# Kernel tuning notes

Measured on AMD Instinct MI355X. Metric: run time of the kernel, lower is better.

## Reference

```python
import jax, jax.numpy as jnp
import numpy as np

N = 50000      # nodes
E = 600000     # edges
D = 128        # num_features == hidden_dim
H = 1          # heads (only runnable config of this module)
C = 128        # per-head channels
L = 2          # num_layers
G = 64         # graphs in batch
NC = 10        # num_classes


def setup_inputs() -> dict:
    key = jax.random.key(0)
    ks = jax.random.split(key, 12)
    s = 1.0 / np.sqrt(D)
    inp = {
        "x": jax.random.normal(ks[0], (N, D), jnp.float32),
        "edge_index": jax.random.randint(ks[1], (2, E), 0, N),
        "batch": jnp.sort(jax.random.randint(ks[2], (N,), 0, G)),
        # per-layer TransformerConv params (stacked over layers)
        "Wq": jax.random.normal(ks[3], (L, D, H * C), jnp.float32) * s,
        "bq": jax.random.normal(ks[4], (L, H * C), jnp.float32) * 0.01,
        "Wk": jax.random.normal(ks[5], (L, D, H * C), jnp.float32) * s,
        "bk": jax.random.normal(ks[6], (L, H * C), jnp.float32) * 0.01,
        "Wv": jax.random.normal(ks[7], (L, D, H * C), jnp.float32) * s,
        "bv": jax.random.normal(ks[8], (L, H * C), jnp.float32) * 0.01,
        "Ws": jax.random.normal(ks[9], (L, D, H * C), jnp.float32) * s,  # lin_skip (root weight)
        "bs": jax.random.normal(ks[10], (L, H * C), jnp.float32) * 0.01,
        "W_fc": jax.random.normal(ks[11], (H * C, NC), jnp.float32) * (1.0 / np.sqrt(H * C)),
        "b_fc": jnp.zeros((NC,), jnp.float32),
    }
    return inp


def _transformer_conv(x, src, dst, wq, bq, wk, bk, wv, bv, ws, bs):
    n = x.shape[0]
    q = (x @ wq + bq).reshape(n, H, C)
    k = (x @ wk + bk).reshape(n, H, C)
    v = (x @ wv + bv).reshape(n, H, C)
    # edge-wise gather: query from dst (x_i), key/value from src (x_j)
    score = (q[dst] * k[src]).sum(-1) / jnp.sqrt(jnp.float32(C))  # [E, H]
    # segment softmax over incoming edges of each dst node
    m = jax.ops.segment_max(score, dst, num_segments=n)           # [N, H]
    ex = jnp.exp(score - m[dst])
    den = jax.ops.segment_sum(ex, dst, num_segments=n)
    alpha = ex / den[dst]                                         # [E, H]
    agg = jax.ops.segment_sum(alpha[..., None] * v[src], dst, num_segments=n)
    return agg.reshape(n, H * C) + x @ ws + bs                    # concat heads + skip


def reference(x, edge_index, batch, Wq, bq, Wk, bk, Wv, bv, Ws, bs, W_fc, b_fc):
    src, dst = edge_index[0], edge_index[1]
    h = x
    for l in range(L):
        h = jax.nn.relu(_transformer_conv(h, src, dst, Wq[l], bq[l], Wk[l], bk[l],
                                          Wv[l], bv[l], Ws[l], bs[l]))
    # global mean pool per graph
    sums = jax.ops.segment_sum(h, batch, num_segments=G)
    cnts = jax.ops.segment_sum(jnp.ones((h.shape[0],), h.dtype), batch, num_segments=G)
    pooled = sums / jnp.maximum(cnts, 1.0)[:, None]
    logits = pooled @ W_fc + b_fc
    return jax.nn.log_softmax(logits, axis=1)
```

## Files before the change

### kernel.cpp

```cpp
#include <hip/hip_runtime.h>
#include <math.h>

#define NN 50000
#define EE 600000
#define DD 128
#define GG 64
#define NCLS 10
#define PCHUNK 64
#define NTILE (NN / 16)
#define NBUK 196
#define BSTRIDE 4096
#define EPB ((EE + 255) / 256)

typedef __attribute__((ext_vector_type(8))) __bf16 bf16x8;
typedef __attribute__((ext_vector_type(8))) unsigned short u16x8;
typedef __attribute__((ext_vector_type(4))) float f32x4;
typedef __attribute__((ext_vector_type(2))) float f32x2;

#define LGKM_FENCE() asm volatile("s_waitcnt lgkmcnt(0)" ::: "memory")
#define SCHED_FENCE() __builtin_amdgcn_sched_barrier(0)

__device__ __forceinline__ unsigned short f2bf(float f) {
    unsigned int u = __float_as_uint(f);
    u += 0x7fff + ((u >> 16) & 1);
    return (unsigned short)(u >> 16);
}

__device__ __forceinline__ float bf2f(unsigned short h) {
    return __uint_as_float(((unsigned int)h) << 16);
}

__device__ __forceinline__ float lo16(unsigned int u) { return __uint_as_float(u << 16); }
__device__ __forceinline__ float hi16(unsigned int u) { return __uint_as_float(u & 0xffff0000u); }


__global__ __launch_bounds__(256) void prep_kernel(
    const float* __restrict__ wq, const float* __restrict__ wk,
    const float* __restrict__ wv, const float* __restrict__ ws,
    const float* __restrict__ x, unsigned short* __restrict__ xb,
    unsigned short* __restrict__ wt,
    int* __restrict__ bucketcnt, float* __restrict__ gsum) {
    int tid = blockIdx.x * 256 + threadIdx.x;
    int TOT = gridDim.x * 256;
    if (tid < 256) bucketcnt[tid] = 0;
    for (int i = tid; i < GG * DD + GG; i += TOT) gsum[i] = 0.f;
    for (int i = tid; i < 2 * 4 * 16384; i += TOT) {
        int k = i & 127;
        int n = (i >> 7) & 127;
        int lm = i >> 14;
        int l = lm >> 2, m = lm & 3;
        const float* w = (m == 0) ? wq : (m == 1) ? wk : (m == 2) ? wv : ws;
        wt[i] = f2bf(w[l * 16384 + k * 128 + n]);
    }
    for (int i = tid; i < NN * DD / 8; i += TOT) {
        const float* px = x + (size_t)i * 8;
        float4 f0 = *(const float4*)px;
        float4 f1 = *(const float4*)(px + 4);
        u16x8 o;
        o[0] = f2bf(f0.x); o[1] = f2bf(f0.y); o[2] = f2bf(f0.z); o[3] = f2bf(f0.w);
        o[4] = f2bf(f1.x); o[5] = f2bf(f1.y); o[6] = f2bf(f1.z); o[7] = f2bf(f1.w);
        *(u16x8*)(xb + (size_t)i * 8) = o;
    }
}


__global__ __launch_bounds__(1024) void bucket_kernel(
    const int* __restrict__ src, const int* __restrict__ dst,
    int* __restrict__ bucketcnt, int2* __restrict__ bedge) {
    __shared__ int hist[256];
    __shared__ int base[256];
    int t = threadIdx.x;
    if (t < 256) hist[t] = 0;
    __syncthreads();
    int e0 = blockIdx.x * EPB;
    int eend = min(e0 + EPB, EE);

    int b0 = -1, b1 = -1, b2 = -1;
    int sl0 = 0, sl1 = 0, sl2 = 0;
    int s0 = 0, s1 = 0, s2 = 0, d0 = 0, d1 = 0, d2 = 0;
    int i = e0 + t;
    if (i < eend) { d0 = dst[i]; s0 = src[i]; b0 = d0 >> 8; sl0 = atomicAdd(&hist[b0], 1); }
    i += 1024;
    if (i < eend) { d1 = dst[i]; s1 = src[i]; b1 = d1 >> 8; sl1 = atomicAdd(&hist[b1], 1); }
    i += 1024;
    if (i < eend) { d2 = dst[i]; s2 = src[i]; b2 = d2 >> 8; sl2 = atomicAdd(&hist[b2], 1); }
    __syncthreads();

    if (t < 256) {
        int h = hist[t];
        base[t] = h ? atomicAdd(&bucketcnt[t], h) : 0;
    }
    __syncthreads();

    if (b0 >= 0) bedge[b0 * BSTRIDE + base[b0] + sl0] = make_int2(s0, d0);
    if (b1 >= 0) bedge[b1 * BSTRIDE + base[b1] + sl1] = make_int2(s1, d1);
    if (b2 >= 0) bedge[b2 * BSTRIDE + base[b2] + sl2] = make_int2(s2, d2);
}


__global__ __launch_bounds__(1024) void bsort_kernel(
    const int* __restrict__ bucketcnt, const int2* __restrict__ bedge,
    int* __restrict__ indptr, int* __restrict__ esrc) {
    __shared__ int buf[256];
    __shared__ int cur[256];
    int b = blockIdx.x;
    int t = threadIdx.x;

    if (t < 256) buf[t] = (t < NBUK) ? bucketcnt[t] : 0;
    __syncthreads();
    if (t < 64) {
        int carry = 0;
        #pragma unroll
        for (int c = 0; c < 4; ++c) {
            int v = buf[c * 64 + t];
            int x = v;
            #pragma unroll
            for (int off = 1; off < 64; off <<= 1) {
                int y = __shfl_up(x, off);
                if (t >= off) x += y;
            }
            cur[c * 64 + t] = carry + x - v;
            carry += __shfl(x, 63);
        }
    }
    __syncthreads();
    int count = buf[b];
    int bstart = cur[b];
    int node0 = b << 8;
    int nn = min(256, NN - node0);
    if (b == 0 && t == 0) indptr[NN] = EE;
    __syncthreads();
    if (t < 256) buf[t] = 0;
    __syncthreads();

    const int2* be = bedge + (size_t)b * BSTRIDE;
    for (int i2 = t; i2 < count; i2 += 1024)
        atomicAdd(&buf[be[i2].y - node0], 1);
    __syncthreads();

    if (t < 64) {
        int carry = 0;
        #pragma unroll
        for (int c = 0; c < 4; ++c) {
            int v = buf[c * 64 + t];
            int x = v;
            #pragma unroll
            for (int off = 1; off < 64; off <<= 1) {
                int y = __shfl_up(x, off);
                if (t >= off) x += y;
            }
            cur[c * 64 + t] = carry + x - v;
            carry += __shfl(x, 63);
        }
    }
    __syncthreads();
    if (t < nn) indptr[node0 + t] = bstart + cur[t];
    __syncthreads();

    for (int i2 = t; i2 < count; i2 += 1024) {
        int2 e = be[i2];
        int slot = atomicAdd(&cur[e.y - node0], 1);
        esrc[bstart + slot] = e.x;
    }
}


__global__ __launch_bounds__(256, 2) void gemm_mfma(
    const unsigned short* __restrict__ xin,
    const unsigned short* __restrict__ wt,
    const float* __restrict__ bq, const float* __restrict__ bk,
    const float* __restrict__ bv, const float* __restrict__ bs,
    unsigned short* __restrict__ qb, unsigned short* __restrict__ sb,
    unsigned char* __restrict__ kv8) {
    __shared__ __align__(16) unsigned short stg[2][16][136];

    int wid = threadIdx.x >> 6;
    int lane = threadIdx.x & 63;
    int typeB = blockIdx.x & 1;
    int mi = wid >> 1;
    int ch = wid & 1;
    int mat = typeB ? (mi ? 2 : 1) : (mi ? 3 : 0);
    int wseq = blockIdx.x >> 1;
    int lr = lane & 15, quad = lane >> 4;

    const unsigned short* wm_ = wt + mat * 16384;
    const float* bias = (mat == 0) ? bq : (mat == 1) ? bk : (mat == 2) ? bv : bs;

    bf16x8 bfr[4][4];
    #pragma unroll
    for (int ks = 0; ks < 4; ++ks)
        #pragma unroll
        for (int tn = 0; tn < 4; ++tn)
            bfr[ks][tn] = *(const bf16x8*)(wm_ + (ch * 64 + tn * 16 + lr) * 128
                                               + ks * 32 + quad * 8);
    float bcol[4];
    #pragma unroll
    for (int tn = 0; tn < 4; ++tn) bcol[tn] = bias[ch * 64 + tn * 16 + lr];

    int t = threadIdx.x;
    int rr = t >> 4;
    int cj = t & 15;

    bf16x8 bufA[4], bufB[4];

    auto load_t = [&](bf16x8 (&b)[4], int tl) {
        const unsigned short* p = xin + (size_t)(tl * 16 + lr) * DD + quad * 8;
        #pragma unroll
        for (int ks = 0; ks < 4; ++ks)
            b[ks] = *(const bf16x8*)(p + ks * 32);
    };

    auto compute_store = [&](bf16x8 (&b)[4], int tile) {
        int row0 = tile * 16;
        f32x4 acc[4];
        #pragma unroll
        for (int tn = 0; tn < 4; ++tn) acc[tn] = (f32x4){0.f, 0.f, 0.f, 0.f};
        #pragma unroll
        for (int ks = 0; ks < 4; ++ks)
            #pragma unroll
            for (int tn = 0; tn < 4; ++tn)
                acc[tn] = __builtin_amdgcn_mfma_f32_16x16x32_bf16(
                    b[ks], bfr[ks][tn], acc[tn], 0, 0, 0);

        #pragma unroll
        for (int tn = 0; tn < 4; ++tn)
            #pragma unroll
            for (int r = 0; r < 4; ++r)
                stg[mi][quad * 4 + r][ch * 64 + tn * 16 + lr] = f2bf(acc[tn][r] + bcol[tn]);
        SCHED_FENCE();
        LGKM_FENCE();
        __builtin_amdgcn_s_barrier();
        SCHED_FENCE();

        if (!typeB) {
            uint4 vq = *(const uint4*)&stg[0][rr][cj * 8];
            *(uint4*)(qb + (size_t)(row0 + rr) * 128 + cj * 8) = vq;
            uint4 vs = *(const uint4*)&stg[1][rr][cj * 8];
            *(uint4*)(sb + (size_t)(row0 + rr) * 128 + cj * 8) = vs;
        } else {
            uint4 kk = *(const uint4*)&stg[0][rr][cj * 8];
            uint4 vv = *(const uint4*)&stg[1][rr][cj * 8];
            unsigned int w0 = __builtin_amdgcn_cvt_pk_fp8_f32(lo16(kk.x), hi16(kk.x), 0, false);
            w0 = __builtin_amdgcn_cvt_pk_fp8_f32(lo16(kk.y), hi16(kk.y), w0, true);
            unsigned int w1 = __builtin_amdgcn_cvt_pk_fp8_f32(lo16(kk.z), hi16(kk.z), 0, false);
            w1 = __builtin_amdgcn_cvt_pk_fp8_f32(lo16(kk.w), hi16(kk.w), w1, true);
            unsigned int w2 = __builtin_amdgcn_cvt_pk_fp8_f32(lo16(vv.x), hi16(vv.x), 0, false);
            w2 = __builtin_amdgcn_cvt_pk_fp8_f32(lo16(vv.y), hi16(vv.y), w2, true);
            unsigned int w3 = __builtin_amdgcn_cvt_pk_fp8_f32(lo16(vv.z), hi16(vv.z), 0, false);
            w3 = __builtin_amdgcn_cvt_pk_fp8_f32(lo16(vv.w), hi16(vv.w), w3, true);
            *(uint4*)(kv8 + (size_t)(row0 + rr) * 256 + cj * 16) = make_uint4(w0, w1, w2, w3);
        }
        SCHED_FENCE();
        LGKM_FENCE();
        __builtin_amdgcn_s_barrier();
        SCHED_FENCE();
    };

    int tile = wseq;
    load_t(bufA, tile);
    for (;;) {
        int t2 = tile + 256;
        if (t2 < NTILE) load_t(bufB, t2);
        compute_store(bufA, tile);
        if (t2 >= NTILE) break;
        tile = t2;
        int t3 = tile + 256;
        if (t3 < NTILE) load_t(bufA, t3);
        compute_store(bufB, tile);
        if (t3 >= NTILE) break;
        tile = t3;
    }
}


__global__ __launch_bounds__(256) void attn_kernel(
    const unsigned short* __restrict__ qb, const unsigned char* __restrict__ kv8,
    const unsigned short* __restrict__ sb,
    const int* __restrict__ indptr, const int* __restrict__ esrc,
    unsigned short* __restrict__ hout, int n) {
    int node = (int)((blockIdx.x * blockDim.x + threadIdx.x) >> 6);
    int lane = threadIdx.x & 63;
    if (node >= n) return;
    int g = lane >> 4, j = lane & 15;

    u16x8 q8 = *(const u16x8*)(qb + (size_t)node * DD + j * 8);
    f32x2 qf2[4];
    #pragma unroll
    for (int c = 0; c < 4; ++c)
        qf2[c] = (f32x2){bf2f(q8[2 * c]), bf2f(q8[2 * c + 1])};

    int beg = indptr[node], end = indptr[node + 1];

    float m = -3.0e38f, den = 0.f;
    f32x2 acc2[4];
    #pragma unroll
    for (int c = 0; c < 4; ++c) acc2[c] = (f32x2){0.f, 0.f};

    int e = beg + g;
    if (e < end) {
        int sidx = esrc[e];
        int en = e + 4;
        int sn = (en < end) ? esrc[en] : 0;
        uint4 kv = *(const uint4*)(kv8 + (size_t)sidx * 256 + j * 16);
        for (;;) {
            bool haven = en < end;
            int en2 = en + 4;
            int sn2 = (en2 < end) ? esrc[en2] : 0;
            uint4 kvn;
            if (haven)
                kvn = *(const uint4*)(kv8 + (size_t)sn * 256 + j * 16);
            f32x2 k01 = __builtin_amdgcn_cvt_pk_f32_fp8(kv.x, false);
            f32x2 k23 = __builtin_amdgcn_cvt_pk_f32_fp8(kv.x, true);
            f32x2 k45 = __builtin_amdgcn_cvt_pk_f32_fp8(kv.y, false);
            f32x2 k67 = __builtin_amdgcn_cvt_pk_f32_fp8(kv.y, true);
            f32x2 p2 = k01 * qf2[0];
            p2 = k23 * qf2[1] + p2;
            p2 = k45 * qf2[2] + p2;
            p2 = k67 * qf2[3] + p2;
            float p_ = p2.x + p2.y;
            p_ += __shfl_xor(p_, 8);
            p_ += __shfl_xor(p_, 4);
            p_ += __shfl_xor(p_, 2);
            p_ += __shfl_xor(p_, 1);
            float score = p_ * 0.088388347648318447f;
            float td = score - m;
            bool up = td >= 0.f;
            float ef = __expf(-fabsf(td));
            float scale = up ? ef : 1.0f;
            float pe = up ? 1.0f : ef;
            if (up) m = score;
            den = fmaf(den, scale, pe);
            f32x2 sc2 = (f32x2){scale, scale};
            f32x2 pe2 = (f32x2){pe, pe};
            f32x2 v01 = __builtin_amdgcn_cvt_pk_f32_fp8(kv.z, false);
            f32x2 v23 = __builtin_amdgcn_cvt_pk_f32_fp8(kv.z, true);
            f32x2 v45 = __builtin_amdgcn_cvt_pk_f32_fp8(kv.w, false);
            f32x2 v67 = __builtin_amdgcn_cvt_pk_f32_fp8(kv.w, true);
            acc2[0] = acc2[0] * sc2 + pe2 * v01;
            acc2[1] = acc2[1] * sc2 + pe2 * v23;
            acc2[2] = acc2[2] * sc2 + pe2 * v45;
            acc2[3] = acc2[3] * sc2 + pe2 * v67;
            if (!haven) break;
            en = en2; sn = sn2; kv = kvn;
        }
    }

    float mo = __shfl_xor(m, 16);
    float m2 = fmaxf(m, mo);
    mo = __shfl_xor(m2, 32);
    float mf = fmaxf(m2, mo);
    float sc = __expf(m - mf);
    den *= sc;
    den += __shfl_xor(den, 16);
    den += __shfl_xor(den, 32);
    float accf[8];
    #pragma unroll
    for (int c = 0; c < 4; ++c) { accf[2 * c] = acc2[c].x; accf[2 * c + 1] = acc2[c].y; }
    #pragma unroll
    for (int c = 0; c < 8; ++c) {
        float a = accf[c] * sc;
        a += __shfl_xor(a, 16);
        a += __shfl_xor(a, 32);
        accf[c] = a;
    }
    float inv = den > 0.f ? 1.0f / den : 0.f;
    if (g == 0) {
        u16x8 s8 = *(const u16x8*)(sb + (size_t)node * DD + j * 8);
        u16x8 o8;
        #pragma unroll
        for (int c = 0; c < 8; ++c)
            o8[c] = f2bf(fmaxf(fmaf(accf[c], inv, bf2f(s8[c])), 0.f));
        *(u16x8*)(hout + (size_t)node * DD + j * 8) = o8;
    }
}


__global__ __launch_bounds__(128) void pool_kernel(const unsigned short* __restrict__ h,
                                                   const int* __restrict__ batch,
                                                   float* __restrict__ gsum,
                                                   float* __restrict__ gcnt, int n) {
    __shared__ int bsh[PCHUNK];
    int t = threadIdx.x;
    int node0 = blockIdx.x * PCHUNK;
    int nnodes = min(PCHUNK, n - node0);
    if (t < nnodes) bsh[t] = batch[node0 + t];
    __syncthreads();

    int cur = bsh[0];
    float acc = 0.f;
    int cnt = 0;
    for (int j0 = 0; j0 < nnodes; j0 += 4) {
        int jm = min(4, nnodes - j0);
        float v[4];
        #pragma unroll
        for (int u = 0; u < 4; ++u)
            v[u] = (u < jm) ? bf2f(h[(size_t)(node0 + j0 + u) * DD + t]) : 0.f;
        #pragma unroll
        for (int u = 0; u < 4; ++u) {
            if (u < jm) {
                int g = bsh[j0 + u];
                if (g != cur) {
                    atomicAdd(&gsum[cur * DD + t], acc);
                    if (t == 0) atomicAdd(&gcnt[cur], (float)cnt);
                    acc = 0.f; cnt = 0; cur = g;
                }
                acc += v[u]; ++cnt;
            }
        }
    }
    if (cnt > 0) {
        atomicAdd(&gsum[cur * DD + t], acc);
        if (t == 0) atomicAdd(&gcnt[cur], (float)cnt);
    }
}


__global__ __launch_bounds__(64) void head_kernel(
    const float* __restrict__ gsum, const float* __restrict__ gcnt,
    const float* __restrict__ wfc, const float* __restrict__ bfc,
    float* __restrict__ out) {
    int g = blockIdx.x;
    int lane = threadIdx.x;
    float cnt = fmaxf(gcnt[g], 1.0f);
    float inv = 1.0f / cnt;
    float p0 = gsum[g * DD + lane] * inv;
    float p1 = gsum[g * DD + lane + 64] * inv;
    __shared__ float logits[NCLS];
    for (int c = 0; c < NCLS; ++c) {
        float partial = p0 * wfc[lane * NCLS + c] + p1 * wfc[(lane + 64) * NCLS + c];
        partial += __shfl_xor(partial, 32);
        partial += __shfl_xor(partial, 16);
        partial += __shfl_xor(partial, 8);
        partial += __shfl_xor(partial, 4);
        partial += __shfl_xor(partial, 2);
        partial += __shfl_xor(partial, 1);
        if (lane == 0) logits[c] = partial + bfc[c];
    }
    __syncthreads();
    if (lane == 0) {
        float mx = logits[0];
        for (int c = 1; c < NCLS; ++c) mx = fmaxf(mx, logits[c]);
        float sum = 0.f;
        for (int c = 0; c < NCLS; ++c) sum += expf(logits[c] - mx);
        float lse = mx + logf(sum);
        for (int c = 0; c < NCLS; ++c) out[g * NCLS + c] = logits[c] - lse;
    }
}


extern "C" void kernel_launch(void* const* d_in, const int* in_sizes, int n_in,
                              void* d_out, int out_size, void* d_ws, size_t ws_size,
                              hipStream_t stream) {
    const float* x     = (const float*)d_in[0];
    const int*   ei    = (const int*)d_in[1];
    const int*   batch = (const int*)d_in[2];
    const float* Wq = (const float*)d_in[3];
    const float* bq = (const float*)d_in[4];
    const float* Wk = (const float*)d_in[5];
    const float* bk = (const float*)d_in[6];
    const float* Wv = (const float*)d_in[7];
    const float* bv = (const float*)d_in[8];
    const float* Ws = (const float*)d_in[9];
    const float* bs = (const float*)d_in[10];
    const float* Wfc = (const float*)d_in[11];
    const float* bfc = (const float*)d_in[12];
    float* out = (float*)d_out;

    const size_t ND = (size_t)NN * DD;
    unsigned short* hbuf = (unsigned short*)d_ws;
    unsigned short* qb  = hbuf + ND;
    unsigned short* sb  = qb + ND;
    unsigned short* wt  = sb + ND;
    unsigned char*  kv8 = (unsigned char*)(wt + 2 * 4 * 16384);
    unsigned short* xb  = (unsigned short*)(kv8 + (size_t)NN * 256);
    int* bucketcnt = (int*)(xb + ND);
    int* indptr    = bucketcnt + 256;
    int* esrc      = indptr + NN + 1;
    int2* bedge    = (int2*)(esrc + EE);
    float* gsum = (float*)(bedge + NBUK * BSTRIDE);
    float* gcnt = gsum + GG * DD;

    const int* src = ei;
    const int* dst = ei + EE;

    prep_kernel<<<512, 256, 0, stream>>>(Wq, Wk, Wv, Ws, x, xb, wt, bucketcnt, gsum);
    bucket_kernel<<<256, 1024, 0, stream>>>(src, dst, bucketcnt, bedge);
    bsort_kernel<<<NBUK, 1024, 0, stream>>>(bucketcnt, bedge, indptr, esrc);

    for (int l = 0; l < 2; ++l) {
        size_t bo = (size_t)l * DD;
        const unsigned short* wtl = wt + (size_t)l * 4 * 16384;
        gemm_mfma<<<512, 256, 0, stream>>>(
            (l == 0) ? xb : hbuf, wtl, bq + bo, bk + bo, bv + bo, bs + bo,
            qb, sb, kv8);
        attn_kernel<<<(NN + 3) / 4, 256, 0, stream>>>(
            qb, kv8, sb, indptr, esrc, hbuf, NN);
    }

    pool_kernel<<<(NN + PCHUNK - 1) / PCHUNK, 128, 0, stream>>>(hbuf, batch, gsum, gcnt, NN);
    head_kernel<<<GG, 64, 0, stream>>>(gsum, gcnt, Wfc, bfc, out);
}
```

Baseline: 249.4 us.

## Deepen attention gather prefetch, prescale query, and double GEMM grid

```diff
diff --git a/kernel.cpp b/kernel.cpp
--- a/kernel.cpp
+++ b/kernel.cpp
@@ -181,6 +181,7 @@
     int ch = wid & 1;
     int mat = typeB ? (mi ? 2 : 1) : (mi ? 3 : 0);
     int wseq = blockIdx.x >> 1;
+    int wstride = gridDim.x >> 1;
     int lr = lane & 15, quad = lane >> 4;
 
     const unsigned short* wm_ = wt + mat * 16384;
@@ -259,12 +260,12 @@
     int tile = wseq;
     load_t(bufA, tile);
     for (;;) {
-        int t2 = tile + 256;
+        int t2 = tile + wstride;
         if (t2 < NTILE) load_t(bufB, t2);
         compute_store(bufA, tile);
         if (t2 >= NTILE) break;
         tile = t2;
-        int t3 = tile + 256;
+        int t3 = tile + wstride;
         if (t3 < NTILE) load_t(bufA, t3);
         compute_store(bufB, tile);
         if (t3 >= NTILE) break;
@@ -284,10 +285,11 @@
     int g = lane >> 4, j = lane & 15;
 
     u16x8 q8 = *(const u16x8*)(qb + (size_t)node * DD + j * 8);
+    const float qsc = 0.088388347648318447f;
     f32x2 qf2[4];
     #pragma unroll
     for (int c = 0; c < 4; ++c)
-        qf2[c] = (f32x2){bf2f(q8[2 * c]), bf2f(q8[2 * c + 1])};
+        qf2[c] = (f32x2){bf2f(q8[2 * c]) * qsc, bf2f(q8[2 * c + 1]) * qsc};
 
     int beg = indptr[node], end = indptr[node + 1];
 
@@ -298,21 +300,24 @@
 
     int e = beg + g;
     if (e < end) {
-        int sidx = esrc[e];
-        int en = e + 4;
-        int sn = (en < end) ? esrc[en] : 0;
-        uint4 kv = *(const uint4*)(kv8 + (size_t)sidx * 256 + j * 16);
+        int s0 = esrc[e];
+        uint4 kv0 = *(const uint4*)(kv8 + (size_t)s0 * 256 + j * 16);
+        int e1 = e + 4;
+        bool h1 = e1 < end;
+        int s1 = h1 ? esrc[e1] : 0;
+        uint4 kv1;
+        if (h1) kv1 = *(const uint4*)(kv8 + (size_t)s1 * 256 + j * 16);
         for (;;) {
-            bool haven = en < end;
-            int en2 = en + 4;
-            int sn2 = (en2 < end) ? esrc[en2] : 0;
-            uint4 kvn;
-            if (haven)
-                kvn = *(const uint4*)(kv8 + (size_t)sn * 256 + j * 16);
-            f32x2 k01 = __builtin_amdgcn_cvt_pk_f32_fp8(kv.x, false);
-            f32x2 k23 = __builtin_amdgcn_cvt_pk_f32_fp8(kv.x, true);
-            f32x2 k45 = __builtin_amdgcn_cvt_pk_f32_fp8(kv.y, false);
-            f32x2 k67 = __builtin_amdgcn_cvt_pk_f32_fp8(kv.y, true);
+            int e2 = e1 + 4;
+            bool h2 = e2 < end;
+            int s2 = h2 ? esrc[e2] : 0;
+            uint4 kv2;
+            if (h2) kv2 = *(const uint4*)(kv8 + (size_t)s2 * 256 + j * 16);
+
+            f32x2 k01 = __builtin_amdgcn_cvt_pk_f32_fp8(kv0.x, false);
+            f32x2 k23 = __builtin_amdgcn_cvt_pk_f32_fp8(kv0.x, true);
+            f32x2 k45 = __builtin_amdgcn_cvt_pk_f32_fp8(kv0.y, false);
+            f32x2 k67 = __builtin_amdgcn_cvt_pk_f32_fp8(kv0.y, true);
             f32x2 p2 = k01 * qf2[0];
             p2 = k23 * qf2[1] + p2;
             p2 = k45 * qf2[2] + p2;
@@ -322,7 +327,7 @@
             p_ += __shfl_xor(p_, 4);
             p_ += __shfl_xor(p_, 2);
             p_ += __shfl_xor(p_, 1);
-            float score = p_ * 0.088388347648318447f;
+            float score = p_;
             float td = score - m;
             bool up = td >= 0.f;
             float ef = __expf(-fabsf(td));
@@ -332,16 +337,19 @@
             den = fmaf(den, scale, pe);
             f32x2 sc2 = (f32x2){scale, scale};
             f32x2 pe2 = (f32x2){pe, pe};
-            f32x2 v01 = __builtin_amdgcn_cvt_pk_f32_fp8(kv.z, false);
-            f32x2 v23 = __builtin_amdgcn_cvt_pk_f32_fp8(kv.z, true);
-            f32x2 v45 = __builtin_amdgcn_cvt_pk_f32_fp8(kv.w, false);
-            f32x2 v67 = __builtin_amdgcn_cvt_pk_f32_fp8(kv.w, true);
+            f32x2 v01 = __builtin_amdgcn_cvt_pk_f32_fp8(kv0.z, false);
+            f32x2 v23 = __builtin_amdgcn_cvt_pk_f32_fp8(kv0.z, true);
+            f32x2 v45 = __builtin_amdgcn_cvt_pk_f32_fp8(kv0.w, false);
+            f32x2 v67 = __builtin_amdgcn_cvt_pk_f32_fp8(kv0.w, true);
             acc2[0] = acc2[0] * sc2 + pe2 * v01;
             acc2[1] = acc2[1] * sc2 + pe2 * v23;
             acc2[2] = acc2[2] * sc2 + pe2 * v45;
             acc2[3] = acc2[3] * sc2 + pe2 * v67;
-            if (!haven) break;
-            en = en2; sn = sn2; kv = kvn;
+
+            if (!h1) break;
+            kv0 = kv1;
+            if (h2) kv1 = kv2;
+            e1 = e2; h1 = h2;
         }
     }
 
@@ -490,7 +498,7 @@
     for (int l = 0; l < 2; ++l) {
         size_t bo = (size_t)l * DD;
         const unsigned short* wtl = wt + (size_t)l * 4 * 16384;
-        gemm_mfma<<<512, 256, 0, stream>>>(
+        gemm_mfma<<<1024, 256, 0, stream>>>(
             (l == 0) ? xb : hbuf, wtl, bq + bo, bk + bo, bv + bo, bs + bo,
             qb, sb, kv8);
         attn_kernel<<<(NN + 3) / 4, 256, 0, stream>>>(
```

Measured after the change: 262.6 us. 1.05x slower.

## Fuse input prep and edge bucketing into one launch with block-role split

Applied to the files above, without the earlier changes.

```diff
diff --git a/kernel.cpp b/kernel.cpp
--- a/kernel.cpp
+++ b/kernel.cpp
@@ -10,7 +10,9 @@
 #define NTILE (NN / 16)
 #define NBUK 196
 #define BSTRIDE 4096
-#define EPB ((EE + 255) / 256)
+#define PBLK 512
+#define BBLK 768
+#define EPB2 ((EE + BBLK - 1) / BBLK)
 
 typedef __attribute__((ext_vector_type(8))) __bf16 bf16x8;
 typedef __attribute__((ext_vector_type(8))) unsigned short u16x8;
@@ -34,67 +36,67 @@
 __device__ __forceinline__ float hi16(unsigned int u) { return __uint_as_float(u & 0xffff0000u); }
 
 
-__global__ __launch_bounds__(256) void prep_kernel(
+__global__ __launch_bounds__(256) void prep_bucket_kernel(
     const float* __restrict__ wq, const float* __restrict__ wk,
     const float* __restrict__ wv, const float* __restrict__ ws,
     const float* __restrict__ x, unsigned short* __restrict__ xb,
-    unsigned short* __restrict__ wt,
-    int* __restrict__ bucketcnt, float* __restrict__ gsum) {
-    int tid = blockIdx.x * 256 + threadIdx.x;
-    int TOT = gridDim.x * 256;
-    if (tid < 256) bucketcnt[tid] = 0;
-    for (int i = tid; i < GG * DD + GG; i += TOT) gsum[i] = 0.f;
-    for (int i = tid; i < 2 * 4 * 16384; i += TOT) {
-        int k = i & 127;
-        int n = (i >> 7) & 127;
-        int lm = i >> 14;
-        int l = lm >> 2, m = lm & 3;
-        const float* w = (m == 0) ? wq : (m == 1) ? wk : (m == 2) ? wv : ws;
-        wt[i] = f2bf(w[l * 16384 + k * 128 + n]);
-    }
-    for (int i = tid; i < NN * DD / 8; i += TOT) {
-        const float* px = x + (size_t)i * 8;
-        float4 f0 = *(const float4*)px;
-        float4 f1 = *(const float4*)(px + 4);
-        u16x8 o;
-        o[0] = f2bf(f0.x); o[1] = f2bf(f0.y); o[2] = f2bf(f0.z); o[3] = f2bf(f0.w);
-        o[4] = f2bf(f1.x); o[5] = f2bf(f1.y); o[6] = f2bf(f1.z); o[7] = f2bf(f1.w);
-        *(u16x8*)(xb + (size_t)i * 8) = o;
-    }
-}
-
-
-__global__ __launch_bounds__(1024) void bucket_kernel(
+    unsigned short* __restrict__ wt, float* __restrict__ gsum,
     const int* __restrict__ src, const int* __restrict__ dst,
     int* __restrict__ bucketcnt, int2* __restrict__ bedge) {
     __shared__ int hist[256];
     __shared__ int base[256];
-    int t = threadIdx.x;
-    if (t < 256) hist[t] = 0;
-    __syncthreads();
-    int e0 = blockIdx.x * EPB;
-    int eend = min(e0 + EPB, EE);
-
-    int b0 = -1, b1 = -1, b2 = -1;
-    int sl0 = 0, sl1 = 0, sl2 = 0;
-    int s0 = 0, s1 = 0, s2 = 0, d0 = 0, d1 = 0, d2 = 0;
-    int i = e0 + t;
-    if (i < eend) { d0 = dst[i]; s0 = src[i]; b0 = d0 >> 8; sl0 = atomicAdd(&hist[b0], 1); }
-    i += 1024;
-    if (i < eend) { d1 = dst[i]; s1 = src[i]; b1 = d1 >> 8; sl1 = atomicAdd(&hist[b1], 1); }
-    i += 1024;
-    if (i < eend) { d2 = dst[i]; s2 = src[i]; b2 = d2 >> 8; sl2 = atomicAdd(&hist[b2], 1); }
-    __syncthreads();
-
-    if (t < 256) {
+
+    if (blockIdx.x < PBLK) {
+        int tid = blockIdx.x * 256 + threadIdx.x;
+        int TOT = PBLK * 256;
+        for (int i = tid; i < GG * DD + GG; i += TOT) gsum[i] = 0.f;
+        for (int i = tid; i < 2 * 4 * 16384; i += TOT) {
+            int k = i & 127;
+            int n = (i >> 7) & 127;
+            int lm = i >> 14;
+            int l = lm >> 2, m = lm & 3;
+            const float* w = (m == 0) ? wq : (m == 1) ? wk : (m == 2) ? wv : ws;
+            wt[i] = f2bf(w[l * 16384 + k * 128 + n]);
+        }
+        for (int i = tid; i < NN * DD / 8; i += TOT) {
+            const float* px = x + (size_t)i * 8;
+            float4 f0 = *(const float4*)px;
+            float4 f1 = *(const float4*)(px + 4);
+            u16x8 o;
+            o[0] = f2bf(f0.x); o[1] = f2bf(f0.y); o[2] = f2bf(f0.z); o[3] = f2bf(f0.w);
+            o[4] = f2bf(f1.x); o[5] = f2bf(f1.y); o[6] = f2bf(f1.z); o[7] = f2bf(f1.w);
+            *(u16x8*)(xb + (size_t)i * 8) = o;
+        }
+    } else {
+        int t = threadIdx.x;
+        hist[t] = 0;
+        __syncthreads();
+        int b = blockIdx.x - PBLK;
+        int e0 = b * EPB2;
+        int eend = min(e0 + EPB2, EE);
+
+        int bk[4], sl[4], es[4], ed[4];
+        #pragma unroll
+        for (int u = 0; u < 4; ++u) {
+            int i = e0 + u * 256 + t;
+            bk[u] = -1;
+            if (i < eend) {
+                ed[u] = dst[i]; es[u] = src[i];
+                bk[u] = ed[u] >> 8;
+                sl[u] = atomicAdd(&hist[bk[u]], 1);
+            }
+        }
+        __syncthreads();
+
         int h = hist[t];
         base[t] = h ? atomicAdd(&bucketcnt[t], h) : 0;
-    }
-    __syncthreads();
-
-    if (b0 >= 0) bedge[b0 * BSTRIDE + base[b0] + sl0] = make_int2(s0, d0);
-    if (b1 >= 0) bedge[b1 * BSTRIDE + base[b1] + sl1] = make_int2(s1, d1);
-    if (b2 >= 0) bedge[b2 * BSTRIDE + base[b2] + sl2] = make_int2(s2, d2);
+        __syncthreads();
+
+        #pragma unroll
+        for (int u = 0; u < 4; ++u)
+            if (bk[u] >= 0)
+                bedge[bk[u] * BSTRIDE + base[bk[u]] + sl[u]] = make_int2(es[u], ed[u]);
+    }
 }
 
 
@@ -483,8 +485,9 @@
     const int* src = ei;
     const int* dst = ei + EE;
 
-    prep_kernel<<<512, 256, 0, stream>>>(Wq, Wk, Wv, Ws, x, xb, wt, bucketcnt, gsum);
-    bucket_kernel<<<256, 1024, 0, stream>>>(src, dst, bucketcnt, bedge);
+    hipMemsetAsync(bucketcnt, 0, 256 * sizeof(int), stream);
+    prep_bucket_kernel<<<PBLK + BBLK, 256, 0, stream>>>(
+        Wq, Wk, Wv, Ws, x, xb, wt, gsum, src, dst, bucketcnt, bedge);
     bsort_kernel<<<NBUK, 1024, 0, stream>>>(bucketcnt, bedge, indptr, esrc);
 
     for (int l = 0; l < 2; ++l) {
```

New measurement: 255.9 us. +2.6%, slower.
